# Kernel tuning notes

Measured on AMD Instinct MI355X. Metric: run time of the kernel, lower is better.

## Reference

```python
import jax, jax.numpy as jnp
import numpy as np

K = 1024   # num_embeddings
E = 64     # embedding_dim
T = 1024   # time
B = 64     # batch
BETA = 0.25  # commitment_cost


def setup_inputs() -> dict:
    key = jax.random.key(0)
    k1, k2 = jax.random.split(key)
    inputs = jax.random.normal(k1, (E, T, B), dtype=jnp.float32)
    # torch init: uniform(-1/num_embeddings, 1/num_embeddings)
    codebook = jax.random.uniform(k2, (K, E), dtype=jnp.float32,
                                  minval=-1.0 / K, maxval=1.0 / K)
    return {"inputs": inputs, "codebook": codebook}


def reference(inputs, codebook):
    # inputs: [E, T, B]; torch does permute(1,2,0) -> [T, B, E]
    x = jnp.transpose(inputs, (1, 2, 0))            # [T, B, E]
    flat = x.reshape(-1, E)                          # [N, E], N = T*B
    d = (jnp.sum(flat * flat, axis=1, keepdims=True)
         + jnp.sum(codebook * codebook, axis=1)
         - 2.0 * (flat @ codebook.T))
    idx = jnp.argmin(d, axis=1)                      # [N]
    # one-hot @ codebook == gather (same math, efficient form)
    q = codebook[idx].reshape(T, B, E)               # [T, B, E]

    e_latent_loss = jnp.mean((jax.lax.stop_gradient(q) - x) ** 2)
    q_latent_loss = jnp.mean((q - jax.lax.stop_gradient(x)) ** 2)
    vq_loss = q_latent_loss + BETA * e_latent_loss

    # straight-through estimator
    q_st = x + jax.lax.stop_gradient(q - x)

    # perplexity from code-usage histogram (mean of one-hots)
    N = flat.shape[0]
    counts = jnp.zeros((K,), jnp.float32).at[idx].add(1.0)
    avg_probs = counts / N
    perplexity = jnp.exp(-jnp.sum(avg_probs * jnp.log(avg_probs + 1e-10)))

    quantized = jnp.transpose(q_st, (2, 0, 1))       # back to [E, T, B]
    return vq_loss, quantized, perplexity
```

## Files before the change

kernel.cpp:

```cpp
#include <hip/hip_runtime.h>


#define KC 1024
#define ED 64
#define NR 65536
#define NE (NR * ED)
#define GAP1 6e-6f

typedef __attribute__((ext_vector_type(8))) short short8;
typedef __attribute__((ext_vector_type(4))) float f32x4;

__device__ __forceinline__ unsigned short bf16rne(float f) {
    unsigned u = __builtin_bit_cast(unsigned, f);
    return (unsigned short)((u + 0x7fffu + ((u >> 16) & 1u)) >> 16);
}
__device__ __forceinline__ float bf16tof(unsigned short h) {
    return __builtin_bit_cast(float, (unsigned)h << 16);
}

__global__ __launch_bounds__(256) void k_pack(const float* __restrict__ cb,
        short8* __restrict__ cbt, unsigned* __restrict__ counts,
        unsigned* __restrict__ flagcnt) {
    const int u = blockIdx.x * 256 + threadIdx.x;
    if (u < 1024) counts[u] = 0u;
    if (u == 1024) *flagcnt = 0u;
    if (u >= 64 * 5 * 64) return;
    const int t = u / 320, rem = u % 320, j = rem / 64, l = rem % 64;
    const int g = l >> 4;
    if (j < 4) {
        const int code = t * 16 + (l & 15);
        const float* c = cb + (size_t)code * ED;
        const bool lo = (j >= 2);
        short8 o;
#pragma unroll
        for (int r = 0; r < 8; ++r) {
            const int e = (j & 1) * 32 + g * 8 + r;
            const float m2 = -2.f * c[e];
            const unsigned short h = bf16rne(m2);
            o[r] = lo ? (short)bf16rne(m2 - bf16tof(h)) : (short)h;
        }
        cbt[u] = o;
    } else {
        f32x4 o;
#pragma unroll
        for (int r = 0; r < 4; ++r) {
            const float4* c4 = (const float4*)(cb + (size_t)(t * 16 + g * 4 + r) * ED);
            float s0 = 0.f, s1 = 0.f, s2 = 0.f, s3 = 0.f;
#pragma unroll
            for (int i = 0; i < 16; ++i) {
                const float4 c = c4[i];
                s0 = fmaf(c.x, c.x, s0); s1 = fmaf(c.y, c.y, s1);
                s2 = fmaf(c.z, c.z, s2); s3 = fmaf(c.w, c.w, s3);
            }
            o[r] = (s0 + s1) + (s2 + s3);
        }
        cbt[u] = __builtin_bit_cast(short8, o);
    }
}

__global__ __launch_bounds__(256) void k_argmin(
        const float* __restrict__ in, const short8* __restrict__ cbt,
        const float* __restrict__ cb, int* __restrict__ idx,
        float* __restrict__ qout, unsigned* __restrict__ counts,
        unsigned* __restrict__ flagcnt, unsigned* __restrict__ flaglist,
        double* __restrict__ pblk) {
    __shared__ short8 xs[16][64];
    __shared__ float rx2p[4][64];
    __shared__ float sb[4][4][16], sb2[4][4][16];
    __shared__ int   sk[4][4][16];
    __shared__ int   fidx[64];

    const int tid = threadIdx.x;
    const int l = tid & 63;
    const int wid = tid >> 6;
    const int g = l >> 4;
    const int col = l & 15;
    const int rowBase = blockIdx.x * 64;

    {
        const int row = tid & 63;
        const int ob = tid >> 6;
        const int rt = row >> 4;
        const int ll = ob * 16 + (row & 15);
        float part = 0.f;
#pragma unroll
        for (int hh = 0; hh < 2; ++hh) {
            short8 H, L;
#pragma unroll
            for (int j = 0; j < 8; ++j) {
                const float x = in[(size_t)(hh * 32 + ob * 8 + j) * NR + rowBase + row];
                const unsigned short hb = bf16rne(x);
                H[j] = (short)hb;
                L[j] = (short)bf16rne(x - bf16tof(hb));
                part = fmaf(x, x, part);
            }
            xs[rt * 4 + hh][ll] = H;
            xs[rt * 4 + 2 + hh][ll] = L;
        }
        rx2p[ob][row] = part;
    }
    __syncthreads();

    const int kh = wid;
    short8 xq[4][4];
#pragma unroll
    for (int rt = 0; rt < 4; ++rt)
#pragma unroll
        for (int q = 0; q < 4; ++q)
            xq[rt][q] = xs[rt * 4 + q][l];

    float best[4]  = {3.4e38f, 3.4e38f, 3.4e38f, 3.4e38f};
    float best2[4] = {3.4e38f, 3.4e38f, 3.4e38f, 3.4e38f};
    int bestk[4] = {0, 0, 0, 0};

#pragma unroll 2
    for (int tt = 0; tt < 16; ++tt) {
        const int t = kh * 16 + tt;
        const short8* bp = cbt + (size_t)t * 320 + l;
        const short8 b0 = bp[0], b1 = bp[64], b2 = bp[128], b3 = bp[192];
        const f32x4 e4 = __builtin_bit_cast(f32x4, bp[256]);
#pragma unroll
        for (int rt = 0; rt < 4; ++rt) {
            f32x4 acc = e4;
            acc = __builtin_amdgcn_mfma_f32_16x16x32_bf16(b0, xq[rt][0], acc, 0, 0, 0);
            acc = __builtin_amdgcn_mfma_f32_16x16x32_bf16(b1, xq[rt][1], acc, 0, 0, 0);
            acc = __builtin_amdgcn_mfma_f32_16x16x32_bf16(b2, xq[rt][0], acc, 0, 0, 0);
            acc = __builtin_amdgcn_mfma_f32_16x16x32_bf16(b3, xq[rt][1], acc, 0, 0, 0);
            acc = __builtin_amdgcn_mfma_f32_16x16x32_bf16(b0, xq[rt][2], acc, 0, 0, 0);
            acc = __builtin_amdgcn_mfma_f32_16x16x32_bf16(b1, xq[rt][3], acc, 0, 0, 0);
#pragma unroll
            for (int r = 0; r < 4; ++r) {
                const float v = acc[r];
                const int k = t * 16 + g * 4 + r;
                best2[rt] = fminf(fmaxf(v, best[rt]), best2[rt]);
                const bool c = v < best[rt];
                bestk[rt] = c ? k : bestk[rt];
                best[rt]  = fminf(v, best[rt]);
            }
        }
    }

#pragma unroll
    for (int rt = 0; rt < 4; ++rt) {
        float b = best[rt], b2 = best2[rt]; int k = bestk[rt];
#pragma unroll
        for (int sh = 16; sh <= 32; sh <<= 1) {
            const float ob  = __shfl_xor(b, sh, 64);
            const float ob2 = __shfl_xor(b2, sh, 64);
            const int   ok  = __shfl_xor(k, sh, 64);
            if (ob < b || (ob == b && ok < k)) { b2 = fminf(b, ob2); k = ok; b = ob; }
            else b2 = fminf(b2, ob);
        }
        if (g == 0) { sb[wid][rt][col] = b; sb2[wid][rt][col] = b2; sk[wid][rt][col] = k; }
    }
    __syncthreads();

    if (wid == 0) {
        const int rt = l >> 4, c2 = l & 15;
        float b = sb[0][rt][c2], b2 = sb2[0][rt][c2]; int k = sk[0][rt][c2];
#pragma unroll
        for (int s = 1; s < 4; ++s) {
            const float ob = sb[s][rt][c2], ob2 = sb2[s][rt][c2];
            const int ok = sk[s][rt][c2];
            if (ob < b || (ob == b && ok < k)) { b2 = fminf(b, ob2); k = ok; b = ob; }
            else b2 = fminf(b2, ob);
        }
        const int lrow = rt * 16 + c2;
        const int row = rowBase + lrow;
        idx[row] = k;
        fidx[lrow] = k;
        atomicAdd(&counts[k], 1u);
        if (b2 - b < GAP1) {
            const unsigned p = atomicAdd(flagcnt, 1u);
            flaglist[p] = (unsigned)row;
        }
        double d2 = (double)b + (double)((rx2p[0][lrow] + rx2p[1][lrow])
                                       + (rx2p[2][lrow] + rx2p[3][lrow]));
#pragma unroll
        for (int off = 32; off > 0; off >>= 1) d2 += __shfl_down(d2, off, 64);
        if (l == 0) pblk[blockIdx.x] = d2;
    }
    __syncthreads();

    {
        const int row = tid & 63;
        const int e0 = tid >> 6;
        const int k = fidx[row];
        const float4* c4 = (const float4*)(cb + (size_t)k * ED + e0 * 16);
#pragma unroll
        for (int j = 0; j < 4; ++j) {
            const float4 v = c4[j];
            qout[(size_t)(e0 * 16 + j * 4 + 0) * NR + rowBase + row] = v.x;
            qout[(size_t)(e0 * 16 + j * 4 + 1) * NR + rowBase + row] = v.y;
            qout[(size_t)(e0 * 16 + j * 4 + 2) * NR + rowBase + row] = v.z;
            qout[(size_t)(e0 * 16 + j * 4 + 3) * NR + rowBase + row] = v.w;
        }
    }
}

__global__ __launch_bounds__(256) void k_exact64(
        const float* __restrict__ in, const float* __restrict__ cb,
        int* __restrict__ idx, float* __restrict__ qout,
        unsigned* __restrict__ counts,
        const unsigned* __restrict__ flagcnt, const unsigned* __restrict__ flaglist) {
    const unsigned nf = *flagcnt;
    const int l = threadIdx.x & 63;
    const unsigned wave = blockIdx.x * 4u + (unsigned)(threadIdx.x >> 6);
    const unsigned nwave = gridDim.x * 4u;
    for (unsigned i = wave; i < nf; i += nwave) {
        const int row = (int)flaglist[i];
        float x[ED];
#pragma unroll
        for (int e = 0; e < ED; ++e) x[e] = in[(size_t)e * NR + row];
        double best = 1e300; int bestk = 0;
        for (int ci = 0; ci < 16; ++ci) {
            const int k = ci * 64 + l;
            const float* c = cb + (size_t)k * ED;
            double s = 0.0, e2 = 0.0;
            for (int e = 0; e < ED; ++e) {
                const double cv = (double)c[e];
                e2 = fma(cv, cv, e2);
                s  = fma(cv, (double)x[e], s);
            }
            const double t = fma(-2.0, s, e2);
            if (t < best) { best = t; bestk = k; }
        }
        for (int sh = 1; sh < 64; sh <<= 1) {
            const double ob = __shfl_xor(best, sh, 64);
            const int   ok  = __shfl_xor(bestk, sh, 64);
            if (ob < best || (ob == best && ok < bestk)) { best = ob; bestk = ok; }
        }
        const int old = idx[row];
        if (bestk != old) {
            if (l == 0) {
                idx[row] = bestk;
                atomicSub(&counts[old], 1u);
                atomicAdd(&counts[bestk], 1u);
            }
            qout[(size_t)l * NR + row] = cb[(size_t)bestk * ED + l];
        }
    }
}

__global__ __launch_bounds__(1024) void k_final(const unsigned* __restrict__ counts,
        const double* __restrict__ pblk, float* __restrict__ out) {
    __shared__ double redE[16], redS[16];
    const int tid = threadIdx.x;
    const double p = (double)counts[tid] * (1.0 / 65536.0);
    double term = p * log(p + 1e-10);
    double s = pblk[tid];
#pragma unroll
    for (int off = 32; off > 0; off >>= 1) {
        term += __shfl_down(term, off, 64);
        s    += __shfl_down(s,    off, 64);
    }
    if ((tid & 63) == 0) { redE[tid >> 6] = term; redS[tid >> 6] = s; }
    __syncthreads();
    if (tid == 0) {
        double e = 0.0, ss = 0.0;
        for (int i = 0; i < 16; ++i) { e += redE[i]; ss += redS[i]; }
        out[1 + NE] = (float)exp(-e);
        const double m = ss * (1.0 / 4194304.0);
        out[0] = (float)(1.25 * m);
    }
}

extern "C" void kernel_launch(void* const* d_in, const int* in_sizes, int n_in,
                              void* d_out, int out_size, void* d_ws, size_t ws_size,
                              hipStream_t stream) {
    (void)in_sizes; (void)n_in; (void)out_size; (void)ws_size;
    const float* in = (const float*)d_in[0];
    const float* cb = (const float*)d_in[1];
    float* out = (float*)d_out;

    unsigned* counts   = (unsigned*)d_ws;
    unsigned* flagcnt  = (unsigned*)d_ws + 1024;
    short8*   cbt      = (short8*)((float*)d_ws + 2048);
    int*      idx      = (int*)d_ws + 83968;
    unsigned* flaglist = (unsigned*)d_ws + 149504;
    double*   pblk     = (double*)((char*)d_ws + 860160);

    hipLaunchKernelGGL(k_pack,    dim3(80),   dim3(256),  0, stream,
                       cb, cbt, counts, flagcnt);
    hipLaunchKernelGGL(k_argmin,  dim3(1024), dim3(256),  0, stream,
                       in, cbt, cb, idx, out + 1, counts, flagcnt, flaglist, pblk);
    hipLaunchKernelGGL(k_exact64, dim3(128),  dim3(256),  0, stream,
                       in, cb, idx, out + 1, counts, flagcnt, flaglist);
    hipLaunchKernelGGL(k_final,   dim3(1),    dim3(1024), 0, stream,
                       counts, pblk, out);
}
```

Before: 79.33 us.

## Halve rows per argmin block and fold final reduction into exact kernel

Each k_argmin block now handles 32 rows instead of 64, so the grid doubles to 2048 blocks. The goal is more parallelism and better latency hiding across the CUs. The cost is that every codebook tile is reloaded for only two row tiles instead of four, which halves codebook reuse per block. Separately, the k_final launch is removed: the last k_exact64 block, found with a done counter and threadfence, computes perplexity and loss, saving one kernel launch.

```diff
diff --git a/kernel.cpp b/kernel.cpp
--- a/kernel.cpp
+++ b/kernel.cpp
@@ -20,10 +20,11 @@
 
 __global__ __launch_bounds__(256) void k_pack(const float* __restrict__ cb,
         short8* __restrict__ cbt, unsigned* __restrict__ counts,
-        unsigned* __restrict__ flagcnt) {
+        unsigned* __restrict__ flagcnt, unsigned* __restrict__ done) {
     const int u = blockIdx.x * 256 + threadIdx.x;
     if (u < 1024) counts[u] = 0u;
     if (u == 1024) *flagcnt = 0u;
+    if (u == 1025) *done = 0u;
     if (u >= 64 * 5 * 64) return;
     const int t = u / 320, rem = u % 320, j = rem / 64, l = rem % 64;
     const int g = l >> 4;
@@ -64,54 +65,52 @@
         float* __restrict__ qout, unsigned* __restrict__ counts,
         unsigned* __restrict__ flagcnt, unsigned* __restrict__ flaglist,
         double* __restrict__ pblk) {
-    __shared__ short8 xs[16][64];
-    __shared__ float rx2p[4][64];
-    __shared__ float sb[4][4][16], sb2[4][4][16];
-    __shared__ int   sk[4][4][16];
-    __shared__ int   fidx[64];
+    __shared__ short8 xs[8][64];
+    __shared__ float rx2p[8][32];
+    __shared__ float sb[4][2][16], sb2[4][2][16];
+    __shared__ int   sk[4][2][16];
+    __shared__ int   fidx[32];
 
     const int tid = threadIdx.x;
     const int l = tid & 63;
     const int wid = tid >> 6;
     const int g = l >> 4;
     const int col = l & 15;
-    const int rowBase = blockIdx.x * 64;
+    const int rowBase = blockIdx.x * 32;
 
     {
-        const int row = tid & 63;
-        const int ob = tid >> 6;
+        const int row = tid & 31;
+        const int ob = tid >> 5;
+        const int hh = ob >> 2, gg = ob & 3;
         const int rt = row >> 4;
-        const int ll = ob * 16 + (row & 15);
+        const int ll = gg * 16 + (row & 15);
         float part = 0.f;
-#pragma unroll
-        for (int hh = 0; hh < 2; ++hh) {
-            short8 H, L;
-#pragma unroll
-            for (int j = 0; j < 8; ++j) {
-                const float x = in[(size_t)(hh * 32 + ob * 8 + j) * NR + rowBase + row];
-                const unsigned short hb = bf16rne(x);
-                H[j] = (short)hb;
-                L[j] = (short)bf16rne(x - bf16tof(hb));
-                part = fmaf(x, x, part);
-            }
-            xs[rt * 4 + hh][ll] = H;
-            xs[rt * 4 + 2 + hh][ll] = L;
-        }
+        short8 H, L;
+#pragma unroll
+        for (int j = 0; j < 8; ++j) {
+            const float x = in[(size_t)(ob * 8 + j) * NR + rowBase + row];
+            const unsigned short hb = bf16rne(x);
+            H[j] = (short)hb;
+            L[j] = (short)bf16rne(x - bf16tof(hb));
+            part = fmaf(x, x, part);
+        }
+        xs[rt * 4 + hh][ll] = H;
+        xs[rt * 4 + 2 + hh][ll] = L;
         rx2p[ob][row] = part;
     }
     __syncthreads();
 
     const int kh = wid;
-    short8 xq[4][4];
-#pragma unroll
-    for (int rt = 0; rt < 4; ++rt)
+    short8 xq[2][4];
+#pragma unroll
+    for (int rt = 0; rt < 2; ++rt)
 #pragma unroll
         for (int q = 0; q < 4; ++q)
             xq[rt][q] = xs[rt * 4 + q][l];
 
-    float best[4]  = {3.4e38f, 3.4e38f, 3.4e38f, 3.4e38f};
-    float best2[4] = {3.4e38f, 3.4e38f, 3.4e38f, 3.4e38f};
-    int bestk[4] = {0, 0, 0, 0};
+    float best[2]  = {3.4e38f, 3.4e38f};
+    float best2[2] = {3.4e38f, 3.4e38f};
+    int bestk[2] = {0, 0};
 
 #pragma unroll 2
     for (int tt = 0; tt < 16; ++tt) {
@@ -120,7 +119,7 @@
         const short8 b0 = bp[0], b1 = bp[64], b2 = bp[128], b3 = bp[192];
         const f32x4 e4 = __builtin_bit_cast(f32x4, bp[256]);
 #pragma unroll
-        for (int rt = 0; rt < 4; ++rt) {
+        for (int rt = 0; rt < 2; ++rt) {
             f32x4 acc = e4;
             acc = __builtin_amdgcn_mfma_f32_16x16x32_bf16(b0, xq[rt][0], acc, 0, 0, 0);
             acc = __builtin_amdgcn_mfma_f32_16x16x32_bf16(b1, xq[rt][1], acc, 0, 0, 0);
@@ -141,7 +140,7 @@
     }
 
 #pragma unroll
-    for (int rt = 0; rt < 4; ++rt) {
+    for (int rt = 0; rt < 2; ++rt) {
         float b = best[rt], b2 = best2[rt]; int k = bestk[rt];
 #pragma unroll
         for (int sh = 16; sh <= 32; sh <<= 1) {
@@ -156,7 +155,8 @@
     __syncthreads();
 
     if (wid == 0) {
-        const int rt = l >> 4, c2 = l & 15;
+        const int rt = (l >> 4) & 1, c2 = l & 15;
+        const bool act = (l < 32);
         float b = sb[0][rt][c2], b2 = sb2[0][rt][c2]; int k = sk[0][rt][c2];
 #pragma unroll
         for (int s = 1; s < 4; ++s) {
@@ -167,34 +167,40 @@
         }
         const int lrow = rt * 16 + c2;
         const int row = rowBase + lrow;
-        idx[row] = k;
-        fidx[lrow] = k;
-        atomicAdd(&counts[k], 1u);
-        if (b2 - b < GAP1) {
-            const unsigned p = atomicAdd(flagcnt, 1u);
-            flaglist[p] = (unsigned)row;
-        }
-        double d2 = (double)b + (double)((rx2p[0][lrow] + rx2p[1][lrow])
-                                       + (rx2p[2][lrow] + rx2p[3][lrow]));
-#pragma unroll
-        for (int off = 32; off > 0; off >>= 1) d2 += __shfl_down(d2, off, 64);
+        double d2 = 0.0;
+        if (act) {
+            idx[row] = k;
+            fidx[lrow] = k;
+            atomicAdd(&counts[k], 1u);
+            if (b2 - b < GAP1) {
+                const unsigned p = atomicAdd(flagcnt, 1u);
+                flaglist[p] = (unsigned)row;
+            }
+            float rx = 0.f;
+#pragma unroll
+            for (int ob2i = 0; ob2i < 8; ++ob2i) rx += rx2p[ob2i][lrow];
+            d2 = (double)b + (double)rx;
+        }
+#pragma unroll
+        for (int off = 16; off > 0; off >>= 1) d2 += __shfl_down(d2, off, 64);
         if (l == 0) pblk[blockIdx.x] = d2;
     }
     __syncthreads();
 
     {
-        const int row = tid & 63;
-        const int e0 = tid >> 6;
+        const int row = tid & 31;
+        const int e0 = tid >> 5;
         const int k = fidx[row];
-        const float4* c4 = (const float4*)(cb + (size_t)k * ED + e0 * 16);
-#pragma unroll
-        for (int j = 0; j < 4; ++j) {
-            const float4 v = c4[j];
-            qout[(size_t)(e0 * 16 + j * 4 + 0) * NR + rowBase + row] = v.x;
-            qout[(size_t)(e0 * 16 + j * 4 + 1) * NR + rowBase + row] = v.y;
-            qout[(size_t)(e0 * 16 + j * 4 + 2) * NR + rowBase + row] = v.z;
-            qout[(size_t)(e0 * 16 + j * 4 + 3) * NR + rowBase + row] = v.w;
-        }
+        const float4* c4 = (const float4*)(cb + (size_t)k * ED + e0 * 8);
+        const float4 v0 = c4[0], v1 = c4[1];
+        qout[(size_t)(e0 * 8 + 0) * NR + rowBase + row] = v0.x;
+        qout[(size_t)(e0 * 8 + 1) * NR + rowBase + row] = v0.y;
+        qout[(size_t)(e0 * 8 + 2) * NR + rowBase + row] = v0.z;
+        qout[(size_t)(e0 * 8 + 3) * NR + rowBase + row] = v0.w;
+        qout[(size_t)(e0 * 8 + 4) * NR + rowBase + row] = v1.x;
+        qout[(size_t)(e0 * 8 + 5) * NR + rowBase + row] = v1.y;
+        qout[(size_t)(e0 * 8 + 6) * NR + rowBase + row] = v1.z;
+        qout[(size_t)(e0 * 8 + 7) * NR + rowBase + row] = v1.w;
     }
 }
 
@@ -202,7 +208,9 @@
         const float* __restrict__ in, const float* __restrict__ cb,
         int* __restrict__ idx, float* __restrict__ qout,
         unsigned* __restrict__ counts,
-        const unsigned* __restrict__ flagcnt, const unsigned* __restrict__ flaglist) {
+        const unsigned* __restrict__ flagcnt, const unsigned* __restrict__ flaglist,
+        unsigned* __restrict__ done, const double* __restrict__ pblk,
+        float* __restrict__ out) {
     const unsigned nf = *flagcnt;
     const int l = threadIdx.x & 63;
     const unsigned wave = blockIdx.x * 4u + (unsigned)(threadIdx.x >> 6);
@@ -240,28 +248,39 @@
             qout[(size_t)l * NR + row] = cb[(size_t)bestk * ED + l];
         }
     }
-}
-
-__global__ __launch_bounds__(1024) void k_final(const unsigned* __restrict__ counts,
-        const double* __restrict__ pblk, float* __restrict__ out) {
-    __shared__ double redE[16], redS[16];
-    const int tid = threadIdx.x;
-    const double p = (double)counts[tid] * (1.0 / 65536.0);
-    double term = p * log(p + 1e-10);
-    double s = pblk[tid];
-#pragma unroll
-    for (int off = 32; off > 0; off >>= 1) {
-        term += __shfl_down(term, off, 64);
-        s    += __shfl_down(s,    off, 64);
-    }
-    if ((tid & 63) == 0) { redE[tid >> 6] = term; redS[tid >> 6] = s; }
-    __syncthreads();
-    if (tid == 0) {
-        double e = 0.0, ss = 0.0;
-        for (int i = 0; i < 16; ++i) { e += redE[i]; ss += redS[i]; }
-        out[1 + NE] = (float)exp(-e);
-        const double m = ss * (1.0 / 4194304.0);
-        out[0] = (float)(1.25 * m);
+
+    __shared__ unsigned isLast;
+    __threadfence();
+    __syncthreads();
+    if (threadIdx.x == 0) isLast = (atomicAdd(done, 1u) == gridDim.x - 1u);
+    __syncthreads();
+    if (isLast) {
+        __threadfence();
+        __shared__ double redE[4], redS[4];
+        const int tid = threadIdx.x;
+        double term = 0.0;
+#pragma unroll
+        for (int i = 0; i < 4; ++i) {
+            const double p = (double)counts[tid + i * 256] * (1.0 / 65536.0);
+            term += p * log(p + 1e-10);
+        }
+        double s = 0.0;
+#pragma unroll
+        for (int i = 0; i < 8; ++i) s += pblk[tid + i * 256];
+#pragma unroll
+        for (int off = 32; off > 0; off >>= 1) {
+            term += __shfl_down(term, off, 64);
+            s    += __shfl_down(s,    off, 64);
+        }
+        if ((tid & 63) == 0) { redE[tid >> 6] = term; redS[tid >> 6] = s; }
+        __syncthreads();
+        if (tid == 0) {
+            const double e = (redE[0] + redE[1]) + (redE[2] + redE[3]);
+            const double ss = (redS[0] + redS[1]) + (redS[2] + redS[3]);
+            out[1 + NE] = (float)exp(-e);
+            const double m = ss * (1.0 / 4194304.0);
+            out[0] = (float)(1.25 * m);
+        }
     }
 }
 
@@ -275,17 +294,17 @@
 
     unsigned* counts   = (unsigned*)d_ws;
     unsigned* flagcnt  = (unsigned*)d_ws + 1024;
+    unsigned* done     = (unsigned*)d_ws + 1025;
     short8*   cbt      = (short8*)((float*)d_ws + 2048);
     int*      idx      = (int*)d_ws + 83968;
     unsigned* flaglist = (unsigned*)d_ws + 149504;
     double*   pblk     = (double*)((char*)d_ws + 860160);
 
-    hipLaunchKernelGGL(k_pack,    dim3(80),   dim3(256),  0, stream,
-                       cb, cbt, counts, flagcnt);
-    hipLaunchKernelGGL(k_argmin,  dim3(1024), dim3(256),  0, stream,
+    hipLaunchKernelGGL(k_pack,    dim3(80),   dim3(256), 0, stream,
+                       cb, cbt, counts, flagcnt, done);
+    hipLaunchKernelGGL(k_argmin,  dim3(2048), dim3(256), 0, stream,
                        in, cbt, cb, idx, out + 1, counts, flagcnt, flaglist, pblk);
-    hipLaunchKernelGGL(k_exact64, dim3(128),  dim3(256),  0, stream,
-                       in, cb, idx, out + 1, counts, flagcnt, flaglist);
-    hipLaunchKernelGGL(k_final,   dim3(1),    dim3(1024), 0, stream,
-                       counts, pblk, out);
-}
+    hipLaunchKernelGGL(k_exact64, dim3(128),  dim3(256), 0, stream,
+                       in, cb, idx, out + 1, counts, flagcnt, flaglist,
+                       done, pblk, out);
+}
```

Result: slower. 89.56 us (+12.9%).
